# Optimization experiments

Hardware: AMD Instinct MI355X
Metric: run time of the kernel (lower is better)

The kernel has to match this reference:

```python
import jax, jax.numpy as jnp
import numpy as np

TEMPERATURE = 0.1
EPS = 1e-06


def setup_inputs() -> dict:
    key = jax.random.key(0)
    k1, k2 = jax.random.split(key)
    N, D = 8192, 256
    z1 = jax.random.normal(k1, (N, D), dtype=jnp.float32)
    z2 = jax.random.normal(k2, (N, D), dtype=jnp.float32)
    return {"z1": z1, "z2": z2}


def reference(z1, z2):
    N = z1.shape[0]
    z = jnp.concatenate([z1, z2], axis=0)                     # (2N, D)
    norm = jnp.maximum(jnp.linalg.norm(z, axis=1, keepdims=True), EPS)
    z_n = z / norm
    sim = jnp.clip(z_n @ z_n.T, -1.0 + EPS, 1.0 - EPS)        # (2N, 2N)
    diag = jnp.arange(N)
    pos_1 = sim[diag, diag + N]
    pos_2 = sim[diag + N, diag]
    positives = jnp.concatenate([pos_1, pos_2])[:, None]      # (2N, 1)
    logits = sim / TEMPERATURE
    eye = jnp.eye(2 * N, dtype=bool)
    logits_masked = jnp.where(eye, -jnp.inf, logits)
    lse = jax.nn.logsumexp(logits_masked, axis=1, keepdims=True)
    loss_per_sample = -positives / TEMPERATURE + lse
    return loss_per_sample.mean()
```

## Files before the change

kernel.cpp:

```cpp
#include <hip/hip_runtime.h>
#include <hip/hip_bf16.h>


typedef __attribute__((ext_vector_type(8)))  short  short8;
typedef __attribute__((ext_vector_type(16))) float  f32x16;
typedef __attribute__((ext_vector_type(4)))  unsigned short u16x4;

#define D 256
#define TEMP_INV 10.0f

typedef __attribute__((address_space(1))) const unsigned int as1_u32;
typedef __attribute__((address_space(3))) unsigned int       as3_u32;

__device__ __forceinline__ void gload_lds16(const void* g, void* l) {
    __builtin_amdgcn_global_load_lds((as1_u32*)g, (as3_u32*)l, 16, 0, 0);
}

__device__ __forceinline__ unsigned short f2bf(float x) {
    unsigned int u = __float_as_uint(x);
    u += 0x7FFFu + ((u >> 16) & 1u);
    return (unsigned short)(u >> 16);
}

__global__ __launch_bounds__(256) void k_norm(const float* __restrict__ z1,
                                              const float* __restrict__ z2,
                                              unsigned short* __restrict__ zn,
                                              float* __restrict__ red, int N) {
    const int wv   = threadIdx.x >> 6;
    const int lane = threadIdx.x & 63;
    const int row  = blockIdx.x * 4 + wv;
    const float* src = (row < N) ? (z1 + (size_t)row * D)
                                 : (z2 + (size_t)(row - N) * D);
    float4 v = *(const float4*)(src + lane * 4);
    float s = v.x * v.x + v.y * v.y + v.z * v.z + v.w * v.w;
    #pragma unroll
    for (int off = 1; off < 64; off <<= 1) s += __shfl_xor(s, off);
    float inv = 1.0f / fmaxf(sqrtf(s), 1e-6f);
    u16x4 o;
    o.x = f2bf(v.x * inv); o.y = f2bf(v.y * inv);
    o.z = f2bf(v.z * inv); o.w = f2bf(v.w * inv);
    *(u16x4*)(zn + (size_t)row * D + lane * 4) = o;

    int tid = blockIdx.x * 256 + threadIdx.x;
    int N2 = 2 * N;
    if (tid <= N2) red[tid] = 0.0f;
}

__global__ __launch_bounds__(512, 2) void k_sim(const unsigned short* __restrict__ zn,
                                                float* __restrict__ rowsum,
                                                float* __restrict__ possum,
                                                int N2) {
    __shared__ __align__(16) char ldsB[2][32768];
    __shared__ float colsum[8][256];

    const int tid  = threadIdx.x;
    const int lane = tid & 63;
    const int w    = tid >> 6;
    const int l31  = lane & 31;
    const int hi   = lane >> 5;

    const int NBr = N2 >> 8;
    const int nwg = (NBr * (NBr + 1)) >> 1;

    const int cpx = nwg >> 3;
    const int bid = (int)blockIdx.x;
    const int p   = (bid & 7) * cpx + (bid >> 3);

    int bi = (int)((2.0f * NBr + 1.0f
                    - sqrtf((float)((2 * NBr + 1) * (2 * NBr + 1) - 8 * p))) * 0.5f);
    while ((bi + 1) * NBr - ((bi + 1) * bi) / 2 <= p) ++bi;
    while (bi * NBr - (bi * (bi - 1)) / 2 > p) --bi;
    const int bj = bi + (p - (bi * NBr - (bi * (bi - 1)) / 2));
    const bool diagWG = (bi == bj);
    const bool posWG  = (bj == bi + (NBr >> 1));

    const int r0 = bi * 256 + w * 32;

    short8 a[16];
    {
        const unsigned short* pA = zn + (size_t)(r0 + l31) * D + hi * 8;
        #pragma unroll
        for (int ks = 0; ks < 16; ++ks) a[ks] = *(const short8*)(pA + ks * 16);
        #pragma unroll
        for (int ks = 0; ks < 16; ++ks) asm volatile("" : "+v"(a[ks]));
    }

    int src_off[4], lds_base[4];
    #pragma unroll
    for (int q = 0; q < 4; ++q) {
        int dl = ((q * 8 + w) * 64 + lane) * 16;
        int row = dl >> 9;
        src_off[q] = dl ^ ((row & 31) << 4);
        lds_base[q] = (q * 8 + w) * 1024;
    }
    const char* Bbase = (const char*)zn + (size_t)bj * 256 * D * 2;

#define STAGE(IT, BUF)                                                        \
    {                                                                         \
        const char* tb_ = Bbase + (IT) * 32768;                               \
        _Pragma("unroll")                                                     \
        for (int q = 0; q < 4; ++q)                                           \
            gload_lds16(tb_ + src_off[q], ldsB[BUF] + lds_base[q]);           \
    }

    float ea[16];
    #pragma unroll
    for (int r = 0; r < 16; ++r) ea[r] = 0.0f;
    float posAcc = 0.0f;

    const float SC   = 14.4269504088896341f;
    const float CLIP = 1.0f - 1e-6f;

    STAGE(0, 0);
    asm volatile("s_waitcnt vmcnt(0)" ::: "memory");
    __builtin_amdgcn_s_barrier();
    __builtin_amdgcn_sched_barrier(0);

    #pragma unroll
    for (int it = 0; it < 4; ++it) {
        const int cur = it & 1;
        if (it == 0) {
            STAGE(1, 1);
        } else {
            if (it < 3) {
                STAGE(it + 1, cur ^ 1);
                asm volatile("s_waitcnt vmcnt(4)" ::: "memory");
            } else {
                asm volatile("s_waitcnt vmcnt(0)" ::: "memory");
            }
            __builtin_amdgcn_s_barrier();
        }
        __builtin_amdgcn_sched_barrier(0);

        f32x16 acc0, acc1;
        #pragma unroll
        for (int r = 0; r < 16; ++r) { acc0[r] = 0.0f; acc1[r] = 0.0f; }

        const char* B = ldsB[cur];
        __builtin_amdgcn_s_setprio(1);
        #pragma unroll
        for (int ks = 0; ks < 16; ++ks) {
            int g = ((((ks << 1) | hi) ^ l31) << 4);
            short8 b0 = *(const short8*)(B + l31 * 512 + g);
            short8 b1 = *(const short8*)(B + (l31 + 32) * 512 + g);
            acc0 = __builtin_amdgcn_mfma_f32_32x32x16_bf16(a[ks], b0, acc0, 0, 0, 0);
            acc1 = __builtin_amdgcn_mfma_f32_32x32x16_bf16(a[ks], b1, acc1, 0, 0, 0);
        }
        __builtin_amdgcn_s_setprio(0);

        float cp0 = 0.0f, cp1 = 0.0f;
        const bool hitW = (diagWG | posWG) && (it == (w >> 1));
        #pragma unroll
        for (int r = 0; r < 16; ++r) {
            float s0 = acc0[r], s1 = acc1[r];
            float e0 = __builtin_amdgcn_exp2f(fmaf(s0, SC, -SC));
            float e1 = __builtin_amdgcn_exp2f(fmaf(s1, SC, -SC));
            if (hitW) {
                int crow = (r & 3) + 8 * (r >> 2) + 4 * hi;
                if (l31 == crow) {
                    if ((w & 1) == 0) {
                        if (diagWG) e0 = 0.0f;
                        else posAcc += 2.0f * fminf(fmaxf(s0, -CLIP), CLIP);
                    } else {
                        if (diagWG) e1 = 0.0f;
                        else posAcc += 2.0f * fminf(fmaxf(s1, -CLIP), CLIP);
                    }
                }
            }
            ea[r] += e0 + e1;
            cp0 += e0;  cp1 += e1;
        }
        if (!diagWG) {
            cp0 += __shfl_xor(cp0, 32);
            cp1 += __shfl_xor(cp1, 32);
            if (lane < 32) {
                colsum[w][it * 64 + l31]      = cp0;
                colsum[w][it * 64 + 32 + l31] = cp1;
            }
        }
        __builtin_amdgcn_s_barrier();
        __builtin_amdgcn_sched_barrier(0);
    }

    __syncthreads();

    #pragma unroll
    for (int r = 0; r < 16; ++r) {
        float v = ea[r];
        v += __shfl_xor(v, 1);  v += __shfl_xor(v, 2);  v += __shfl_xor(v, 4);
        v += __shfl_xor(v, 8);  v += __shfl_xor(v, 16);
        if (l31 == 0)
            atomicAdd(rowsum + r0 + (r & 3) + 8 * (r >> 2) + 4 * hi, v);
    }

    if (!diagWG && tid < 256) {
        float cv = 0.0f;
        #pragma unroll
        for (int w8 = 0; w8 < 8; ++w8) cv += colsum[w8][tid];
        atomicAdd(rowsum + bj * 256 + tid, cv);
    }

    if (posWG) {
        #pragma unroll
        for (int off = 1; off < 64; off <<= 1) posAcc += __shfl_xor(posAcc, off);
        if (lane == 0) atomicAdd(possum, posAcc);
    }
#undef STAGE
}

__global__ __launch_bounds__(1024) void k_final(const float* __restrict__ red,
                                                float* __restrict__ out, int N2) {
    __shared__ float sm[16];
    float s = 0.0f;
    for (int i = threadIdx.x; i < N2; i += 1024)
        s += __logf(red[i]);
    #pragma unroll
    for (int off = 1; off < 64; off <<= 1) s += __shfl_xor(s, off);
    const int wv = threadIdx.x >> 6, lane = threadIdx.x & 63;
    if (lane == 0) sm[wv] = s;
    __syncthreads();
    if (threadIdx.x == 0) {
        float t = 0.0f;
        #pragma unroll
        for (int w = 0; w < 16; ++w) t += sm[w];
        float possum = red[N2];
        out[0] = (t + 10.0f * (float)N2 - possum * TEMP_INV) / (float)N2;
    }
}

extern "C" void kernel_launch(void* const* d_in, const int* in_sizes, int n_in,
                              void* d_out, int out_size, void* d_ws, size_t ws_size,
                              hipStream_t stream) {
    const float* z1 = (const float*)d_in[0];
    const float* z2 = (const float*)d_in[1];
    const int N  = in_sizes[0] / D;
    const int N2 = 2 * N;
    const int NBr = N2 / 256;
    const int nwg = (NBr * (NBr + 1)) / 2;

    unsigned short* zn = (unsigned short*)d_ws;
    float* red = (float*)((char*)d_ws + (size_t)N2 * D * sizeof(unsigned short));

    k_norm<<<N2 / 4, 256, 0, stream>>>(z1, z2, zn, red, N);
    k_sim<<<nwg, 512, 0, stream>>>(zn, red, red + N2, N2);
    k_final<<<1, 1024, 0, stream>>>(red, (float*)d_out, N2);
}
```

Before: 235.9 us.

## Triple-buffer B tiles and remap workgroups to balanced per-XCD block bands

```diff
diff --git a/kernel.cpp b/kernel.cpp
--- a/kernel.cpp
+++ b/kernel.cpp
@@ -50,7 +50,7 @@
                                                 float* __restrict__ rowsum,
                                                 float* __restrict__ possum,
                                                 int N2) {
-    __shared__ __align__(16) char ldsB[2][32768];
+    __shared__ __align__(16) char ldsB[3][32768];
     __shared__ float colsum[8][256];
 
     const int tid  = threadIdx.x;
@@ -59,20 +59,29 @@
     const int l31  = lane & 31;
     const int hi   = lane >> 5;
 
-    const int NBr = N2 >> 8;
-    const int nwg = (NBr * (NBr + 1)) >> 1;
-
-    const int cpx = nwg >> 3;
     const int bid = (int)blockIdx.x;
-    const int p   = (bid & 7) * cpx + (bid >> 3);
-
-    int bi = (int)((2.0f * NBr + 1.0f
-                    - sqrtf((float)((2 * NBr + 1) * (2 * NBr + 1) - 8 * p))) * 0.5f);
-    while ((bi + 1) * NBr - ((bi + 1) * bi) / 2 <= p) ++bi;
-    while (bi * NBr - (bi * (bi - 1)) / 2 > p) --bi;
-    const int bj = bi + (p - (bi * NBr - (bi * (bi - 1)) / 2));
+    const int x   = bid & 7;
+    {
+    }
+    int bi = 0, bj = 0;
+    {
+        const int L0 = 4 * x, H0 = 60 - 4 * x;
+        int s = bid >> 3;
+        for (int b = 0; b < 64; ++b) {
+            int cL = (b < L0) ? 4 : ((b < L0 + 4) ? (L0 + 4 - b) : 0);
+            int cH = (b < H0) ? 4 : ((b < H0 + 4) ? (H0 + 4 - b) : 0);
+            int c  = cL + cH;
+            if (s < c) {
+                bi = b;
+                bj = (s < cL) ? ((b > L0 ? b : L0) + s)
+                              : ((b > H0 ? b : H0) + (s - cL));
+                break;
+            }
+            s -= c;
+        }
+    }
     const bool diagWG = (bi == bj);
-    const bool posWG  = (bj == bi + (NBr >> 1));
+    const bool posWG  = (bj == bi + 32);
 
     const int r0 = bi * 256 + w * 32;
 
@@ -111,32 +120,11 @@
     const float SC   = 14.4269504088896341f;
     const float CLIP = 1.0f - 1e-6f;
 
-    STAGE(0, 0);
-    asm volatile("s_waitcnt vmcnt(0)" ::: "memory");
-    __builtin_amdgcn_s_barrier();
-    __builtin_amdgcn_sched_barrier(0);
-
-    #pragma unroll
-    for (int it = 0; it < 4; ++it) {
-        const int cur = it & 1;
-        if (it == 0) {
-            STAGE(1, 1);
-        } else {
-            if (it < 3) {
-                STAGE(it + 1, cur ^ 1);
-                asm volatile("s_waitcnt vmcnt(4)" ::: "memory");
-            } else {
-                asm volatile("s_waitcnt vmcnt(0)" ::: "memory");
-            }
-            __builtin_amdgcn_s_barrier();
-        }
-        __builtin_amdgcn_sched_barrier(0);
-
+    auto compute_tile = [&](const char* B, int itT) {
         f32x16 acc0, acc1;
         #pragma unroll
         for (int r = 0; r < 16; ++r) { acc0[r] = 0.0f; acc1[r] = 0.0f; }
 
-        const char* B = ldsB[cur];
         __builtin_amdgcn_s_setprio(1);
         #pragma unroll
         for (int ks = 0; ks < 16; ++ks) {
@@ -149,7 +137,7 @@
         __builtin_amdgcn_s_setprio(0);
 
         float cp0 = 0.0f, cp1 = 0.0f;
-        const bool hitW = (diagWG | posWG) && (it == (w >> 1));
+        const bool hitW = (diagWG | posWG) && (itT == (w >> 1));
         #pragma unroll
         for (int r = 0; r < 16; ++r) {
             float s0 = acc0[r], s1 = acc1[r];
@@ -174,13 +162,42 @@
             cp0 += __shfl_xor(cp0, 32);
             cp1 += __shfl_xor(cp1, 32);
             if (lane < 32) {
-                colsum[w][it * 64 + l31]      = cp0;
-                colsum[w][it * 64 + 32 + l31] = cp1;
+                colsum[w][itT * 64 + l31]      = cp0;
+                colsum[w][itT * 64 + 32 + l31] = cp1;
             }
         }
-        __builtin_amdgcn_s_barrier();
-        __builtin_amdgcn_sched_barrier(0);
-    }
+    };
+
+    STAGE(0, 0);
+    STAGE(1, 1);
+    asm volatile("s_waitcnt vmcnt(4)" ::: "memory");
+    __builtin_amdgcn_s_barrier();
+    __builtin_amdgcn_sched_barrier(0);
+
+    STAGE(2, 2);
+    compute_tile(ldsB[0], 0);
+    __builtin_amdgcn_s_barrier();
+    __builtin_amdgcn_sched_barrier(0);
+
+    STAGE(3, 0);
+    asm volatile("s_waitcnt vmcnt(8)" ::: "memory");
+    __builtin_amdgcn_s_barrier();
+    __builtin_amdgcn_sched_barrier(0);
+    compute_tile(ldsB[1], 1);
+    __builtin_amdgcn_s_barrier();
+    __builtin_amdgcn_sched_barrier(0);
+
+    asm volatile("s_waitcnt vmcnt(4)" ::: "memory");
+    __builtin_amdgcn_s_barrier();
+    __builtin_amdgcn_sched_barrier(0);
+    compute_tile(ldsB[2], 2);
+    __builtin_amdgcn_s_barrier();
+    __builtin_amdgcn_sched_barrier(0);
+
+    asm volatile("s_waitcnt vmcnt(0)" ::: "memory");
+    __builtin_amdgcn_s_barrier();
+    __builtin_amdgcn_sched_barrier(0);
+    compute_tile(ldsB[0], 3);
 
     __syncthreads();
 
```

Result: slower. 246.3 us (+4.4%).
